# Optimization experiments

Hardware: AMD Instinct MI355X
Metric: run time of the kernel (lower is better)

## Reference

```python
import jax, jax.numpy as jnp
import numpy as np

B, S, D_MODEL, H, D_SP = 4, 1024, 1024, 16, 512
DEPTH = D_MODEL // H
NEG_INF = -1e9


def setup_inputs() -> dict:
    key = jax.random.key(0)
    ks = jax.random.split(key, 12)
    def dense(kw, kb, fan_in, fan_out):
        lim = (6.0 / (fan_in + fan_out)) ** 0.5  # glorot_uniform
        W = jax.random.uniform(kw, (fan_in, fan_out), jnp.float32, -lim, lim)
        b = jnp.zeros((fan_out,), jnp.float32)
        return W, b
    W_sp, b_sp = dense(ks[0], ks[1], S, D_SP)
    Wq, bq = dense(ks[2], ks[3], D_MODEL, D_MODEL)
    Wk, bk = dense(ks[4], ks[5], D_SP, D_MODEL)
    Wv, bv = dense(ks[6], ks[7], D_SP, D_MODEL)
    Wo, bo = dense(ks[8], ks[9], D_MODEL, D_MODEL)
    q = jax.random.normal(ks[10], (B, S, D_MODEL), jnp.float32)
    min_distance_matrix = jax.random.uniform(ks[11], (B, S, S), jnp.float32)
    mask = jax.random.randint(jax.random.fold_in(key, 7), (B, 1, S, S), 0, 2).astype(jnp.float32)
    return {"q": q, "min_distance_matrix": min_distance_matrix, "mask": mask,
            "W_sp": W_sp, "b_sp": b_sp, "Wq": Wq, "bq": bq, "Wk": Wk, "bk": bk,
            "Wv": Wv, "bv": bv, "Wo": Wo, "bo": bo}


def _split_heads(x):
    # [B,S,d_model] -> [B,H,S,depth]
    return x.reshape(B, S, H, DEPTH).transpose(0, 2, 1, 3)


def reference(q, min_distance_matrix, mask, W_sp, b_sp, Wq, bq, Wk, bk, Wv, bv, Wo, bo):
    # SpatialEncoding: Dense(d_sp_enc, activation='relu') over last axis of [B,S,S]
    sp = jax.nn.relu(min_distance_matrix @ W_sp + b_sp)  # [B,S,d_sp]
    qh = _split_heads(q @ Wq + bq)   # [B,H,S,depth]
    kh = _split_heads(sp @ Wk + bk)
    vh = _split_heads(sp @ Wv + bv)
    scale = jnp.float32(DEPTH) ** -0.5
    logits = jnp.einsum('bhqd,bhkd->bhqk', qh, kh) * scale
    # tf.repeat(mask, H, axis=1): mask [B,1,S,S] broadcast over heads
    logits = logits + mask * NEG_INF
    attn = jax.nn.softmax(logits, axis=-1)               # [B,H,S,S]
    ctx = jnp.einsum('bhqk,bhkd->bhqd', attn, vh)        # [B,H,S,depth]
    concat = ctx.transpose(0, 2, 1, 3).reshape(B, S, D_MODEL)
    out = concat @ Wo + bo
    return out, attn
```

## Files before the change

### kernel.cpp

```cpp
#include <hip/hip_runtime.h>
#include <hip/hip_bf16.h>
#include <cmath>


typedef __bf16 bf16x8 __attribute__((ext_vector_type(8)));
typedef __bf16 bf16x4 __attribute__((ext_vector_type(4)));
typedef float  f32x4  __attribute__((ext_vector_type(4)));

#define MFMA16(a, b, c) __builtin_amdgcn_mfma_f32_16x16x32_bf16((a), (b), (c), 0, 0, 0)

static constexpr int S = 1024, DM = 1024, H = 16, DEPTH = 64;

__device__ inline float wave_max(float v) {
#pragma unroll
  for (int o = 32; o > 0; o >>= 1) v = fmaxf(v, __shfl_xor(v, o));
  return v;
}
__device__ inline float wave_sum(float v) {
#pragma unroll
  for (int o = 32; o > 0; o >>= 1) v += __shfl_xor(v, o);
  return v;
}

__device__ inline bf16x8 cvt8(const float* p) {
  float4 f0 = *reinterpret_cast<const float4*>(p);
  float4 f1 = *reinterpret_cast<const float4*>(p + 4);
  bf16x8 a = {(__bf16)f0.x, (__bf16)f0.y, (__bf16)f0.z, (__bf16)f0.w,
              (__bf16)f1.x, (__bf16)f1.y, (__bf16)f1.z, (__bf16)f1.w};
  return a;
}

__device__ inline void gl_lds16(const __bf16* g, void* l) {
  __builtin_amdgcn_global_load_lds(
      (const __attribute__((address_space(1))) unsigned int*)g,
      (__attribute__((address_space(3))) unsigned int*)l, 16, 0, 0);
}

__device__ inline void tr_body(const float* __restrict__ W, __bf16* __restrict__ WT,
                               int K, int N, int bx, int by) {
  __shared__ float tile[64][65];
  int k0 = bx * 64, n0 = by * 64;
  int t = threadIdx.x;
  int r = t >> 2, c4 = (t & 3) * 16;
  const float* src = W + (size_t)(k0 + r) * N + n0 + c4;
#pragma unroll
  for (int j = 0; j < 4; j++) {
    float4 v = *reinterpret_cast<const float4*>(src + j * 4);
    tile[r][c4 + j * 4 + 0] = v.x;
    tile[r][c4 + j * 4 + 1] = v.y;
    tile[r][c4 + j * 4 + 2] = v.z;
    tile[r][c4 + j * 4 + 3] = v.w;
  }
  __syncthreads();
  __bf16* dst = WT + (size_t)(n0 + r) * K + k0 + c4;
  bf16x8 o0, o1;
#pragma unroll
  for (int j = 0; j < 8; j++) {
    o0[j] = (__bf16)tile[c4 + j][r];
    o1[j] = (__bf16)tile[c4 + 8 + j][r];
  }
  *reinterpret_cast<bf16x8*>(dst) = o0;
  *reinterpret_cast<bf16x8*>(dst + 8) = o1;
}

__global__ __launch_bounds__(256) void prep(
    const float* __restrict__ mdm, const float* __restrict__ q,
    const float* __restrict__ Wsp, const float* __restrict__ Wq,
    const float* __restrict__ Wk, const float* __restrict__ Wv,
    const float* __restrict__ Wo, __bf16* mdm_b, __bf16* q_b, __bf16* WspT,
    __bf16* WqT, __bf16* WkT, __bf16* WvT, __bf16* WoT) {
  int id = blockIdx.x;
  if (id < 4096) {
    int i = id * 256 + threadIdx.x;
    if (i < 524288) {
      *reinterpret_cast<bf16x8*>(mdm_b + (size_t)i * 8) = cvt8(mdm + (size_t)i * 8);
    } else {
      int j = i - 524288;
      *reinterpret_cast<bf16x8*>(q_b + (size_t)j * 8) = cvt8(q + (size_t)j * 8);
    }
    return;
  }
  id -= 4096;
  if (id < 128)      tr_body(Wsp, WspT, 1024, 512, id & 15, id >> 4);
  else if (id < 384) { id -= 128; tr_body(Wq, WqT, 1024, 1024, id & 15, id >> 4); }
  else if (id < 512) { id -= 384; tr_body(Wk, WkT, 512, 1024, id & 7, id >> 3); }
  else if (id < 640) { id -= 512; tr_body(Wv, WvT, 512, 1024, id & 7, id >> 3); }
  else               { id -= 640; tr_body(Wo, WoT, 1024, 1024, id & 15, id >> 4); }
}

template <int K, int MODE, typename OutT>
__global__ __launch_bounds__(512) void gemmL8(const __bf16* __restrict__ A,
                                              const __bf16* __restrict__ A2,
                                              const __bf16* __restrict__ BT,
                                              const __bf16* __restrict__ BT2,
                                              const float* __restrict__ bias,
                                              const float* __restrict__ bias2,
                                              OutT* __restrict__ out,
                                              OutT* __restrict__ out2, int N) {
  __shared__ __bf16 smA[2][128 * 32];
  __shared__ __bf16 smB[2][128 * 32];
  int tid = threadIdx.x, lane = tid & 63, wv = tid >> 6;
  int lr = lane & 15, hi = lane >> 4;
  int wr = (wv >> 2) * 64, wc = (wv & 3) * 32;
  int row0 = blockIdx.y * 128;

  bool is_sp = (MODE == 4) && (blockIdx.x < 4);
  int col0;
  const __bf16 *Abase, *Bbase;
  if (MODE == 4) {
    col0 = is_sp ? blockIdx.x * 128 : (blockIdx.x - 4) * 128;
    Abase = is_sp ? A : A2;
    Bbase = is_sp ? BT : BT2;
  } else {
    col0 = blockIdx.x * 128;
    Abase = A;
    Bbase = BT;
  }

  auto stage = [&](int buf, int k0) {
    int c = tid;
    gl_lds16(Abase + (size_t)(row0 + (c >> 2)) * K + k0 + (c & 3) * 8,
             (char*)smA[buf] + (tid >> 6) * 1024);
    gl_lds16(Bbase + (size_t)(col0 + (c >> 2)) * K + k0 + (c & 3) * 8,
             (char*)smB[buf] + (tid >> 6) * 1024);
  };

  stage(0, 0);
  __syncthreads();

  f32x4 acc[4][2] = {};
  int cur = 0;
  for (int k0 = 32; k0 <= K; k0 += 32) {
    if (k0 < K) stage(cur ^ 1, k0);
    bf16x8 a[4], b[2];
#pragma unroll
    for (int m = 0; m < 4; m++)
      a[m] = *reinterpret_cast<const bf16x8*>(smA[cur] + (wr + m * 16 + lr) * 32 + hi * 8);
#pragma unroll
    for (int n = 0; n < 2; n++)
      b[n] = *reinterpret_cast<const bf16x8*>(smB[cur] + (wc + n * 16 + lr) * 32 + hi * 8);
#pragma unroll
    for (int m = 0; m < 4; m++)
#pragma unroll
      for (int n = 0; n < 2; n++) acc[m][n] = MFMA16(a[m], b[n], acc[m][n]);
    __syncthreads();
    cur ^= 1;
  }

  int rb = hi * 4;
#pragma unroll
  for (int m = 0; m < 4; m++)
#pragma unroll
    for (int n = 0; n < 2; n++) {
      int col = col0 + wc + n * 16 + lr;
      float bia;
      if (MODE == 3) bia = (col >= 1024) ? bias2[col - 1024] : bias[col];
      else if (MODE == 4) bia = is_sp ? bias[col] : bias2[col];
      else bia = bias[col];
#pragma unroll
      for (int r = 0; r < 4; r++) {
        int row = row0 + wr + m * 16 + rb + r;
        float v = acc[m][n][r] + bia;
        if (MODE == 0) {
          out[(size_t)row * N + col] = (OutT)v;
        } else if (MODE == 3) {
          int bb = row >> 10, s = row & 1023;
          if (col < 1024) {
            int h = col >> 6, d = col & 63;
            out[(((size_t)(bb * H + h)) * S + s) * DEPTH + d] = (OutT)v;
          } else {
            int c2 = col - 1024, h = c2 >> 6, d = c2 & 63;
            out2[(((size_t)(bb * H + h)) * DEPTH + d) * S + s] = (OutT)v;
          }
        } else {
          if (is_sp) {
            out[(size_t)row * 512 + col] = (OutT)fmaxf(v, 0.0f);
          } else {
            int bb = row >> 10, s = row & 1023, h = col >> 6, d = col & 63;
            out2[(((size_t)(bb * H + h)) * S + s) * DEPTH + d] = (OutT)v;
          }
        }
      }
    }
}

__global__ __launch_bounds__(256) void attn_fused(const __bf16* __restrict__ qh,
                                                  const __bf16* __restrict__ kh,
                                                  const __bf16* __restrict__ vhT,
                                                  const float* __restrict__ mask,
                                                  float* __restrict__ attn,
                                                  __bf16* __restrict__ concat) {
  __shared__ float4 smem4[2048];
  char* sm = (char*)smem4;
  int lane = threadIdx.x & 63, wv = threadIdx.x >> 6;
  int q0 = blockIdx.x * 16;
  int bh = blockIdx.y;
  int b = bh >> 4, h = bh & 15;
  int lr = lane & 15, hi = lane >> 4, lk = hi * 8;
  int rb = hi * 4;

  const __bf16* qbase = qh + (size_t)bh * S * DEPTH;
  const __bf16* kbase = kh + (size_t)bh * S * DEPTH;
  const __bf16* vbase = vhT + (size_t)bh * DEPTH * S;

  bf16x8 a0 = *reinterpret_cast<const bf16x8*>(qbase + (q0 + lr) * DEPTH + lk);
  bf16x8 a1 = *reinterpret_cast<const bf16x8*>(qbase + (q0 + lr) * DEPTH + 32 + lk);
  int swzq = (lr & 7) << 4;
#pragma unroll 4
  for (int ct = 0; ct < 16; ct++) {
    int col0 = wv * 256 + ct * 16;
    f32x4 acc = {};
    bf16x8 b0 = *reinterpret_cast<const bf16x8*>(kbase + (col0 + lr) * DEPTH + lk);
    bf16x8 b1 = *reinterpret_cast<const bf16x8*>(kbase + (col0 + lr) * DEPTH + 32 + lk);
    acc = MFMA16(b0, a0, acc);
    acc = MFMA16(b1, a1, acc);
    bf16x4 st = {(__bf16)(acc[0] * 0.125f), (__bf16)(acc[1] * 0.125f),
                 (__bf16)(acc[2] * 0.125f), (__bf16)(acc[3] * 0.125f)};
    int byte = lr * 2048 + (((col0 + hi * 4) * 2) ^ swzq);
    *reinterpret_cast<bf16x4*>(sm + byte) = st;
  }
  __syncthreads();

  float* abase = attn + (size_t)bh * S * S + (size_t)q0 * S;
  for (int rr = 0; rr < 4; rr++) {
    int row = wv * 4 + rr;
    int base = row * 2048, swz = (row & 7) << 4;
    const float* mrow = mask + ((size_t)b * S + q0 + row) * S;
    bf16x4 praw[4];
    float4 mk[4];
#pragma unroll
    for (int j = 0; j < 4; j++) {
      praw[j] = *reinterpret_cast<const bf16x4*>(sm + base + ((j * 512 + lane * 8) ^ swz));
      mk[j] = *reinterpret_cast<const float4*>(mrow + j * 256 + lane * 4);
    }
    float v[16];
#pragma unroll
    for (int j = 0; j < 4; j++) {
      v[j * 4 + 0] = (float)praw[j][0] + mk[j].x * (-1e9f);
      v[j * 4 + 1] = (float)praw[j][1] + mk[j].y * (-1e9f);
      v[j * 4 + 2] = (float)praw[j][2] + mk[j].z * (-1e9f);
      v[j * 4 + 3] = (float)praw[j][3] + mk[j].w * (-1e9f);
    }
    float m = v[0];
#pragma unroll
    for (int i = 1; i < 16; i++) m = fmaxf(m, v[i]);
    m = wave_max(m);
    float e[16], ssum = 0.f;
#pragma unroll
    for (int i = 0; i < 16; i++) {
      e[i] = __expf(v[i] - m);
      ssum += e[i];
    }
    ssum = wave_sum(ssum);
    float inv = 1.0f / ssum;
#pragma unroll
    for (int j = 0; j < 4; j++) {
      f32x4 st = {e[j * 4 + 0] * inv, e[j * 4 + 1] * inv, e[j * 4 + 2] * inv, e[j * 4 + 3] * inv};
      __builtin_nontemporal_store(
          st, reinterpret_cast<f32x4*>(abase + (size_t)row * S + j * 256 + lane * 4));
      bf16x4 pw = {(__bf16)st[0], (__bf16)st[1], (__bf16)st[2], (__bf16)st[3]};
      *reinterpret_cast<bf16x4*>(sm + base + ((j * 512 + lane * 8) ^ swz)) = pw;
    }
  }
  __syncthreads();

  f32x4 pacc[4] = {};
  int kw = wv * 256;
#pragma unroll
  for (int step = 0; step < 8; step++) {
    int k0 = kw + step * 32;
    int abyte = lr * 2048 + (((k0 + hi * 8) * 2) ^ swzq);
    bf16x8 a = *reinterpret_cast<const bf16x8*>(sm + abyte);
#pragma unroll
    for (int t = 0; t < 4; t++) {
      bf16x8 bb = *reinterpret_cast<const bf16x8*>(vbase + (size_t)(t * 16 + lr) * S + k0 + lk);
      pacc[t] = MFMA16(a, bb, pacc[t]);
    }
  }
  __syncthreads();

  float* fp = (float*)sm;
#pragma unroll
  for (int t = 0; t < 4; t++)
#pragma unroll
    for (int r = 0; r < 4; r++) fp[wv * 1024 + (rb + r) * 64 + t * 16 + lr] = pacc[t][r];
  __syncthreads();

  int row = threadIdx.x >> 4;
  int c0 = (threadIdx.x & 15) * 4;
  f32x4 sum = {};
#pragma unroll
  for (int w = 0; w < 4; w++) sum += *reinterpret_cast<f32x4*>(&fp[w * 1024 + row * 64 + c0]);
  __bf16* cdst = concat + ((size_t)b * S + q0 + row) * DM + h * DEPTH + c0;
  bf16x4 o = {(__bf16)sum[0], (__bf16)sum[1], (__bf16)sum[2], (__bf16)sum[3]};
  *reinterpret_cast<bf16x4*>(cdst) = o;
}


extern "C" void kernel_launch(void* const* d_in, const int* in_sizes, int n_in,
                              void* d_out, int out_size, void* d_ws, size_t ws_size,
                              hipStream_t stream) {
  const float* q    = (const float*)d_in[0];
  const float* mdm  = (const float*)d_in[1];
  const float* mask = (const float*)d_in[2];
  const float* W_sp = (const float*)d_in[3];
  const float* b_sp = (const float*)d_in[4];
  const float* Wq   = (const float*)d_in[5];
  const float* bq   = (const float*)d_in[6];
  const float* Wk   = (const float*)d_in[7];
  const float* bk   = (const float*)d_in[8];
  const float* Wv   = (const float*)d_in[9];
  const float* bv   = (const float*)d_in[10];
  const float* Wo   = (const float*)d_in[11];
  const float* bo   = (const float*)d_in[12];

  char* p = (char*)d_ws;
  __bf16* WspT   = (__bf16*)p; p += (size_t)524288 * 2;
  __bf16* WkT    = (__bf16*)p; p += (size_t)524288 * 2;
  __bf16* WvT    = (__bf16*)p; p += (size_t)524288 * 2;
  __bf16* WqT    = (__bf16*)p; p += (size_t)1048576 * 2;
  __bf16* WoT    = (__bf16*)p; p += (size_t)1048576 * 2;
  __bf16* sp     = (__bf16*)p; p += (size_t)2097152 * 2;
  __bf16* qh     = (__bf16*)p; p += (size_t)4194304 * 2;
  __bf16* kh     = (__bf16*)p; p += (size_t)4194304 * 2;
  __bf16* vhT    = (__bf16*)p; p += (size_t)4194304 * 2;
  __bf16* concat = (__bf16*)p; p += (size_t)4194304 * 2;
  __bf16* mdm_b  = (__bf16*)p; p += (size_t)4194304 * 2;
  __bf16* q_b    = (__bf16*)p; p += (size_t)4194304 * 2;

  float* out_p  = (float*)d_out;
  float* attn_p = (float*)d_out + (size_t)4194304;

  prep<<<4992, 256, 0, stream>>>(mdm, q, W_sp, Wq, Wk, Wv, Wo,
                                 mdm_b, q_b, WspT, WqT, WkT, WvT, WoT);

  gemmL8<1024, 4, __bf16><<<dim3(12, 32), 512, 0, stream>>>(
      mdm_b, q_b, WspT, WqT, b_sp, bq, sp, qh, 512);

  gemmL8<512, 3, __bf16><<<dim3(16, 32), 512, 0, stream>>>(
      sp, nullptr, WkT, nullptr, bk, bv, kh, vhT, 2048);

  attn_fused<<<dim3(64, 64), 256, 0, stream>>>(qh, kh, vhT, mask, attn_p, concat);

  gemmL8<1024, 0, float><<<dim3(8, 32), 512, 0, stream>>>(
      concat, nullptr, WoT, nullptr, bo, nullptr, out_p, nullptr, 1024);
}
```

Measured before the change: 232.9 us.

## Enlarge attention tile to 32 queries, cast mask to bf16, remap blocks by XCD

The attention kernel now processes 32 query rows per 512-thread block, so each K tile loaded from global memory feeds two query groups. The mask is pre-cast to bf16 in a separate kernel that reuses the mdm_b buffer, which halves the mask bytes read inside attention but adds a full read and write pass over the mask. Blocks are remapped so that the eight heads sharing an XCD are grouped together, improving L2 locality for K and V. The larger block doubles LDS use to 64KB, which may reduce occupancy.

```diff
diff --git a/kernel.cpp b/kernel.cpp
--- a/kernel.cpp
+++ b/kernel.cpp
@@ -86,6 +86,12 @@
   else if (id < 512) { id -= 384; tr_body(Wk, WkT, 512, 1024, id & 7, id >> 3); }
   else if (id < 640) { id -= 512; tr_body(Wv, WvT, 512, 1024, id & 7, id >> 3); }
   else               { id -= 640; tr_body(Wo, WoT, 1024, 1024, id & 15, id >> 4); }
+}
+
+__global__ __launch_bounds__(256) void cast_mask(const float* __restrict__ mask,
+                                                 __bf16* __restrict__ maskb) {
+  int i = blockIdx.x * 256 + threadIdx.x;
+  *reinterpret_cast<bf16x8*>(maskb + (size_t)i * 8) = cvt8(mask + (size_t)i * 8);
 }
 
 template <int K, int MODE, typename OutT>
@@ -184,40 +190,50 @@
     }
 }
 
-__global__ __launch_bounds__(256) void attn_fused(const __bf16* __restrict__ qh,
+__global__ __launch_bounds__(512) void attn_fused(const __bf16* __restrict__ qh,
                                                   const __bf16* __restrict__ kh,
                                                   const __bf16* __restrict__ vhT,
-                                                  const float* __restrict__ mask,
+                                                  const __bf16* __restrict__ maskb,
                                                   float* __restrict__ attn,
                                                   __bf16* __restrict__ concat) {
-  __shared__ float4 smem4[2048];
+  __shared__ float4 smem4[4096];
   char* sm = (char*)smem4;
-  int lane = threadIdx.x & 63, wv = threadIdx.x >> 6;
-  int q0 = blockIdx.x * 16;
-  int bh = blockIdx.y;
-  int b = bh >> 4, h = bh & 15;
+  int tid = threadIdx.x, lane = tid & 63, wv = tid >> 6;
   int lr = lane & 15, hi = lane >> 4, lk = hi * 8;
   int rb = hi * 4;
+
+  int lin = blockIdx.y * 32 + blockIdx.x;
+  int xcd = lin & 7, idx = lin >> 3;
+  int bh = xcd * 8 + (idx >> 5);
+  int q0 = (idx & 31) * 32;
+  int b = bh >> 4, h = bh & 15;
 
   const __bf16* qbase = qh + (size_t)bh * S * DEPTH;
   const __bf16* kbase = kh + (size_t)bh * S * DEPTH;
   const __bf16* vbase = vhT + (size_t)bh * DEPTH * S;
 
-  bf16x8 a0 = *reinterpret_cast<const bf16x8*>(qbase + (q0 + lr) * DEPTH + lk);
-  bf16x8 a1 = *reinterpret_cast<const bf16x8*>(qbase + (q0 + lr) * DEPTH + 32 + lk);
+  bf16x8 aq[2][2];
+#pragma unroll
+  for (int qg = 0; qg < 2; qg++) {
+    aq[qg][0] = *reinterpret_cast<const bf16x8*>(qbase + (q0 + qg * 16 + lr) * DEPTH + lk);
+    aq[qg][1] = *reinterpret_cast<const bf16x8*>(qbase + (q0 + qg * 16 + lr) * DEPTH + 32 + lk);
+  }
   int swzq = (lr & 7) << 4;
-#pragma unroll 4
-  for (int ct = 0; ct < 16; ct++) {
-    int col0 = wv * 256 + ct * 16;
-    f32x4 acc = {};
+#pragma unroll 2
+  for (int ct = 0; ct < 8; ct++) {
+    int col0 = wv * 128 + ct * 16;
     bf16x8 b0 = *reinterpret_cast<const bf16x8*>(kbase + (col0 + lr) * DEPTH + lk);
     bf16x8 b1 = *reinterpret_cast<const bf16x8*>(kbase + (col0 + lr) * DEPTH + 32 + lk);
-    acc = MFMA16(b0, a0, acc);
-    acc = MFMA16(b1, a1, acc);
-    bf16x4 st = {(__bf16)(acc[0] * 0.125f), (__bf16)(acc[1] * 0.125f),
-                 (__bf16)(acc[2] * 0.125f), (__bf16)(acc[3] * 0.125f)};
-    int byte = lr * 2048 + (((col0 + hi * 4) * 2) ^ swzq);
-    *reinterpret_cast<bf16x4*>(sm + byte) = st;
+#pragma unroll
+    for (int qg = 0; qg < 2; qg++) {
+      f32x4 acc = {};
+      acc = MFMA16(b0, aq[qg][0], acc);
+      acc = MFMA16(b1, aq[qg][1], acc);
+      bf16x4 st = {(__bf16)(acc[0] * 0.125f), (__bf16)(acc[1] * 0.125f),
+                   (__bf16)(acc[2] * 0.125f), (__bf16)(acc[3] * 0.125f)};
+      int byte = (qg * 16 + lr) * 2048 + (((col0 + hi * 4) * 2) ^ swzq);
+      *reinterpret_cast<bf16x4*>(sm + byte) = st;
+    }
   }
   __syncthreads();
 
@@ -225,22 +241,19 @@
   for (int rr = 0; rr < 4; rr++) {
     int row = wv * 4 + rr;
     int base = row * 2048, swz = (row & 7) << 4;
-    const float* mrow = mask + ((size_t)b * S + q0 + row) * S;
-    bf16x4 praw[4];
-    float4 mk[4];
+    const __bf16* mrow = maskb + ((size_t)b * S + q0 + row) * S;
+    bf16x4 praw[4], mk[4];
 #pragma unroll
     for (int j = 0; j < 4; j++) {
       praw[j] = *reinterpret_cast<const bf16x4*>(sm + base + ((j * 512 + lane * 8) ^ swz));
-      mk[j] = *reinterpret_cast<const float4*>(mrow + j * 256 + lane * 4);
+      mk[j] = *reinterpret_cast<const bf16x4*>(mrow + j * 256 + lane * 4);
     }
     float v[16];
 #pragma unroll
-    for (int j = 0; j < 4; j++) {
-      v[j * 4 + 0] = (float)praw[j][0] + mk[j].x * (-1e9f);
-      v[j * 4 + 1] = (float)praw[j][1] + mk[j].y * (-1e9f);
-      v[j * 4 + 2] = (float)praw[j][2] + mk[j].z * (-1e9f);
-      v[j * 4 + 3] = (float)praw[j][3] + mk[j].w * (-1e9f);
-    }
+    for (int j = 0; j < 4; j++)
+#pragma unroll
+      for (int e = 0; e < 4; e++)
+        v[j * 4 + e] = (float)praw[j][e] + (float)mk[j][e] * (-1e9f);
     float m = v[0];
 #pragma unroll
     for (int i = 1; i < 16; i++) m = fmaxf(m, v[i]);
@@ -264,12 +277,12 @@
   }
   __syncthreads();
 
+  int kc = wv >> 1, rg = wv & 1;
   f32x4 pacc[4] = {};
-  int kw = wv * 256;
 #pragma unroll
   for (int step = 0; step < 8; step++) {
-    int k0 = kw + step * 32;
-    int abyte = lr * 2048 + (((k0 + hi * 8) * 2) ^ swzq);
+    int k0 = kc * 256 + step * 32;
+    int abyte = (rg * 16 + lr) * 2048 + (((k0 + hi * 8) * 2) ^ swzq);
     bf16x8 a = *reinterpret_cast<const bf16x8*>(sm + abyte);
 #pragma unroll
     for (int t = 0; t < 4; t++) {
@@ -283,14 +296,15 @@
 #pragma unroll
   for (int t = 0; t < 4; t++)
 #pragma unroll
-    for (int r = 0; r < 4; r++) fp[wv * 1024 + (rb + r) * 64 + t * 16 + lr] = pacc[t][r];
-  __syncthreads();
-
-  int row = threadIdx.x >> 4;
-  int c0 = (threadIdx.x & 15) * 4;
+    for (int r = 0; r < 4; r++)
+      fp[kc * 2048 + (rg * 16 + rb + r) * 64 + t * 16 + lr] = pacc[t][r];
+  __syncthreads();
+
+  int row = tid >> 4;
+  int c0 = (tid & 15) * 4;
   f32x4 sum = {};
 #pragma unroll
-  for (int w = 0; w < 4; w++) sum += *reinterpret_cast<f32x4*>(&fp[w * 1024 + row * 64 + c0]);
+  for (int w = 0; w < 4; w++) sum += *reinterpret_cast<f32x4*>(&fp[w * 2048 + row * 64 + c0]);
   __bf16* cdst = concat + ((size_t)b * S + q0 + row) * DM + h * DEPTH + c0;
   bf16x4 o = {(__bf16)sum[0], (__bf16)sum[1], (__bf16)sum[2], (__bf16)sum[3]};
   *reinterpret_cast<bf16x4*>(cdst) = o;
@@ -327,6 +341,7 @@
   __bf16* concat = (__bf16*)p; p += (size_t)4194304 * 2;
   __bf16* mdm_b  = (__bf16*)p; p += (size_t)4194304 * 2;
   __bf16* q_b    = (__bf16*)p; p += (size_t)4194304 * 2;
+  __bf16* maskb  = mdm_b;
 
   float* out_p  = (float*)d_out;
   float* attn_p = (float*)d_out + (size_t)4194304;
@@ -337,10 +352,12 @@
   gemmL8<1024, 4, __bf16><<<dim3(12, 32), 512, 0, stream>>>(
       mdm_b, q_b, WspT, WqT, b_sp, bq, sp, qh, 512);
 
+  cast_mask<<<2048, 256, 0, stream>>>(mask, maskb);
+
   gemmL8<512, 3, __bf16><<<dim3(16, 32), 512, 0, stream>>>(
       sp, nullptr, WkT, nullptr, bk, bv, kh, vhT, 2048);
 
-  attn_fused<<<dim3(64, 64), 256, 0, stream>>>(qh, kh, vhT, mask, attn_p, concat);
+  attn_fused<<<dim3(32, 64), 512, 0, stream>>>(qh, kh, vhT, maskb, attn_p, concat);
 
   gemmL8<1024, 0, float><<<dim3(8, 32), 512, 0, stream>>>(
       concat, nullptr, WoT, nullptr, bo, nullptr, out_p, nullptr, 1024);
```

After: 221.6 us. 1.05x faster.
